# Optimization experiments

Hardware: AMD Instinct MI355X
Metric: run time of the kernel (lower is better)

Reference implementation:

```python
import jax, jax.numpy as jnp
import numpy as np

N = 50000            # problem dimension (free subspace)
K = 64               # low-rank dimension of the Hessian model
M = 64               # number of active equality constraints (rows of A)
MAX_CG_ITER = 40     # static bound on CG iterations -> reorth buffer size
CG_TOL = 1e-6
CG_REG = 1e-8
TOL_ABS = 1e-14      # _HRSTCG_TOL_ABS


def setup_inputs() -> dict:
    key = jax.random.key(0)
    k1, k2, k3, k4 = jax.random.split(key, 4)
    g_eff = jax.random.normal(k1, (N,), jnp.float32)
    # SPD diagonal part of the working Hessian: entries in [1, 2)
    diag = jax.random.uniform(k2, (N,), jnp.float32) + 1.0
    # low-rank factor, scaled so U U^T has O(1) spectrum
    U = jax.random.normal(k3, (N, K), jnp.float32) / np.float32(np.sqrt(N))
    # active constraint matrix, scaled so A A^T is well conditioned
    A = jax.random.normal(k4, (M, N), jnp.float32) / np.float32(np.sqrt(N))
    return {"g_eff": g_eff, "diag": diag, "U": U, "A": A}


def _hr_stcg(g_eff, diag, U, A):
    n = g_eff.shape[0]
    dtype = g_eff.dtype
    # exact null-space projector W(v) = v - A^T (A A^T)^{-1} A v
    AAt = A @ A.T + 1e-8 * jnp.eye(A.shape[0], dtype=A.dtype)
    AAt_inv = jnp.linalg.inv(AAt)
    project = lambda v: v - A.T @ (AAt_inv @ (A @ v))
    # working-subspace HVP: H v = diag*v + U (U^T v)  (SPD)
    hvp_work = lambda v: diag * v + U @ (U.T @ v)

    indices = jnp.arange(MAX_CG_ITER)

    Wg = project(g_eff)
    r0 = -Wg
    proj_grad_norm = jnp.sqrt(jnp.maximum(jnp.dot(r0, r0), 0.0))
    rz0 = jnp.dot(r0, r0)  # z0 = r0

    # state: (t, r, z, p, rz, P, HP, pHp_diag, iteration, converged)
    init_state = (
        jnp.zeros(n, dtype), r0, r0, r0, rz0,
        jnp.zeros((MAX_CG_ITER, n), dtype),
        jnp.zeros((MAX_CG_ITER, n), dtype),
        jnp.zeros(MAX_CG_ITER, dtype),
        jnp.array(0),
        jnp.reshape(proj_grad_norm <= TOL_ABS, ()),
    )

    def do_step(s):
        t, r, z, p, rz, P, HP, pHp_diag, it, conv = s
        Hp = hvp_work(p)
        pHp = jnp.dot(p, Hp)
        pp = jnp.dot(p, p)
        abs_floor = CG_REG * proj_grad_norm * proj_grad_norm
        bad_curvature = pHp <= jnp.maximum(CG_REG * pp, abs_floor)
        rp = jnp.dot(r, p)
        stagnation = jnp.abs(rp) < 1e-30
        sc = bad_curvature | stagnation  # short_circuit
        pHp_safe = jnp.maximum(pHp, 1e-30)
        alpha = jnp.where(sc, jnp.asarray(0.0, dtype), rz / pHp_safe)
        t_new = t + alpha * p
        r_new = r - alpha * Hp                 # modified residual recurrence
        z_new = project(r_new)
        P_buf = P.at[it].set(p)
        HP_buf = HP.at[it].set(Hp)
        pHp_buf = pHp_diag.at[it].set(pHp)
        mask_j = indices <= it
        Hz_dots = HP_buf @ z_new               # full H-conjugacy reorth
        pHp_diag_safe = jnp.where(jnp.abs(pHp_buf) > 1e-30, pHp_buf, 1e-30)
        coeffs = jnp.where(mask_j, Hz_dots / pHp_diag_safe, 0.0)
        p_new = z_new - coeffs @ P_buf
        rz_new = jnp.dot(r_new, z_new)
        z_norm = jnp.sqrt(jnp.maximum(jnp.dot(z_new, z_new), 0.0))
        tol_target = jnp.maximum(TOL_ABS, CG_TOL * proj_grad_norm)
        conv_new = (z_norm <= tol_target) | sc
        return (
            jnp.where(sc, t, t_new), jnp.where(sc, r, r_new),
            jnp.where(sc, z, z_new), jnp.where(sc, p, p_new),
            jnp.where(sc, rz, rz_new),
            P_buf, HP_buf, pHp_buf, it + 1, conv_new,
        )

    def step_fn(_i, s):
        return jax.lax.cond(jnp.reshape(s[-1], ()), lambda x: x, do_step, s)

    final = jax.lax.fori_loop(0, MAX_CG_ITER, step_fn, init_state)
    return final[0], proj_grad_norm, final[-1]


def reference(g_eff, diag, U, A):
    # returns (t_k, ||r0||, converged) as in _hr_stcg
    return _hr_stcg(g_eff, diag, U, A)
```

## Files before the change

kernel.cpp:

```cpp
#include <hip/hip_runtime.h>
#include <hip/hip_cooperative_groups.h>
#include <math.h>

namespace cg = cooperative_groups;

#define N_ 50000
#define K_ 64
#define M_ 64
#define MAXIT 40
#define NC 782
#define BSZ 256

#define CG_TOLf  1e-6f
#define CG_REGf  1e-8f
#define TOL_ABSf 1e-14f

#define OFF_AATB 0
#define OFF_INV  16384
#define OFF_S0   20480
#define OFF_AHP  20544
#define OFF_PGN2 23168
#define OFF_Y0   23680
#define OFF_BAR  56448
#define OFF_BUFA 57472
#define OFF_BUFB 230528
#define WS_HEAD  301184
#define OFF_PB   WS_HEAD
#define OFF_HPB  (OFF_PB + MAXIT * N_)

#define BUFA_SZ  86528
#define BUFB_SZ  35328

__device__ __forceinline__ float wred(float v) {
#pragma unroll
  for (int m = 1; m < 64; m <<= 1) v += __shfl_xor(v, m, 64);
  return v;
}

__device__ __forceinline__ void gbar(unsigned* bar, int b, int NB, unsigned ep) {
  __syncthreads();
  if (threadIdx.x == 0) {
    __threadfence();
    const int grp = b & 15;
    const unsigned gsz = (unsigned)((NB - grp + 15) >> 4);
    unsigned o = __hip_atomic_fetch_add(&bar[grp * 32], 1u, __ATOMIC_RELAXED, __HIP_MEMORY_SCOPE_AGENT);
    if (o % gsz == gsz - 1u) {
      unsigned r = __hip_atomic_fetch_add(&bar[16 * 32], 1u, __ATOMIC_RELAXED, __HIP_MEMORY_SCOPE_AGENT);
      if ((r & 15u) == 15u)
        __hip_atomic_fetch_add(&bar[17 * 32], 1u, __ATOMIC_RELEASE, __HIP_MEMORY_SCOPE_AGENT);
    }
    while (__hip_atomic_load(&bar[17 * 32], __ATOMIC_RELAXED, __HIP_MEMORY_SCOPE_AGENT) < ep)
      __builtin_amdgcn_s_sleep(2);
    __threadfence();
  }
  __syncthreads();
}

__device__ __forceinline__ void zslot(float* p, float v) {
  __hip_atomic_store(p, v, __ATOMIC_RELAXED, __HIP_MEMORY_SCOPE_AGENT);
}

__global__ __launch_bounds__(BSZ, 4)
void stcg_kernel(const float* __restrict__ g, const float* __restrict__ dg,
                 const float* __restrict__ U, const float* __restrict__ A,
                 float* __restrict__ out, float* __restrict__ ws)
{
  cg::grid_group grid = cg::this_grid();
  const int b = blockIdx.x, NB = gridDim.x, t = threadIdx.x;
  const int wv = t >> 6, lane = t & 63;
  const int base1 = b * 64;
  const int col1 = base1 + lane;
  const bool valid1 = col1 < N_;
  const bool own2 = (b + NB) < NC;
  const int base2 = (b + NB) * 64;
  const int col2 = base2 + lane;
  const bool valid2 = own2 && (col2 < N_);
  const int nv2 = own2 ? min(64, N_ - base2) : 0;
  const int bank32 = (b & 15) * 32;

  __shared__ float Als[64 * 65];
  __shared__ float Uls[64 * 65];
  __shared__ float partA[BSZ], partB[BSZ];
  __shared__ float rL[64], hpL[64], pL[64];
  __shared__ float rL2[64], hpL2[64], pL2[64];
  __shared__ float wsh[64], ssh[64], gL[64], cshL[64];
  __shared__ float rowk[64], fsh[64];
  __shared__ float redL[176];
  __shared__ float pHpdL[MAXIT];
  __shared__ float scalSh[8];

  float* Pb  = ws + OFF_PB;
  float* HPb = ws + OFF_HPB;
  unsigned* bar = (unsigned*)(ws + OFF_BAR);
  unsigned ep = 0;

  float t_ = 0.f, r_ = 0.f, p_ = 0.f, d_ = 0.f;
  float t2_ = 0.f, r2_ = 0.f, p2_ = 0.f, d2_ = 0.f;
  if (wv == 0 && valid1) d_ = dg[col1];
  if (wv == 1 && valid2) d2_ = dg[col2];

  for (int idx = b * BSZ + t; idx < WS_HEAD; idx += NB * BSZ) ws[idx] = 0.f;
  grid.sync();

  float aat[4][4];
#pragma unroll
  for (int a = 0; a < 4; ++a)
#pragma unroll
    for (int c = 0; c < 4; ++c) aat[a][c] = 0.f;
  const int tr4 = (t >> 4) << 2, tc4 = (t & 15) << 2;

  if (wv == 0) gL[lane] = valid1 ? g[col1] : 0.f;
#pragma unroll
  for (int kk = 0; kk < 16; ++kk) {
    const int m = wv * 16 + kk;
    Als[m * 65 + lane] = valid1 ? A[(size_t)m * N_ + col1] : 0.f;
  }
  __syncthreads();
  {
#pragma unroll 4
    for (int j = 0; j < 64; ++j) {
      float a0 = Als[(tr4 + 0) * 65 + j], a1 = Als[(tr4 + 1) * 65 + j];
      float a2 = Als[(tr4 + 2) * 65 + j], a3 = Als[(tr4 + 3) * 65 + j];
      float b0 = Als[(tc4 + 0) * 65 + j], b1 = Als[(tc4 + 1) * 65 + j];
      float b2 = Als[(tc4 + 2) * 65 + j], b3 = Als[(tc4 + 3) * 65 + j];
      aat[0][0] += a0 * b0; aat[0][1] += a0 * b1; aat[0][2] += a0 * b2; aat[0][3] += a0 * b3;
      aat[1][0] += a1 * b0; aat[1][1] += a1 * b1; aat[1][2] += a1 * b2; aat[1][3] += a1 * b3;
      aat[2][0] += a2 * b0; aat[2][1] += a2 * b1; aat[2][2] += a2 * b2; aat[2][3] += a2 * b3;
      aat[3][0] += a3 * b0; aat[3][1] += a3 * b1; aat[3][2] += a3 * b2; aat[3][3] += a3 * b3;
    }
    if (wv == 0) {
      float s = 0.f;
#pragma unroll 8
      for (int c = 0; c < 64; ++c) s += Als[lane * 65 + c] * gL[c];
      atomicAdd(&ws[OFF_Y0 + lane * 512 + bank32], s);
    }
  }
  if (own2) {
    __syncthreads();
    if (wv == 1) gL[lane] = valid2 ? g[col2] : 0.f;
#pragma unroll
    for (int kk = 0; kk < 16; ++kk) {
      const int m = wv * 16 + kk;
      Als[m * 65 + lane] = valid2 ? A[(size_t)m * N_ + col2] : 0.f;
    }
    __syncthreads();
#pragma unroll 4
    for (int j = 0; j < 64; ++j) {
      float a0 = Als[(tr4 + 0) * 65 + j], a1 = Als[(tr4 + 1) * 65 + j];
      float a2 = Als[(tr4 + 2) * 65 + j], a3 = Als[(tr4 + 3) * 65 + j];
      float b0 = Als[(tc4 + 0) * 65 + j], b1 = Als[(tc4 + 1) * 65 + j];
      float b2 = Als[(tc4 + 2) * 65 + j], b3 = Als[(tc4 + 3) * 65 + j];
      aat[0][0] += a0 * b0; aat[0][1] += a0 * b1; aat[0][2] += a0 * b2; aat[0][3] += a0 * b3;
      aat[1][0] += a1 * b0; aat[1][1] += a1 * b1; aat[1][2] += a1 * b2; aat[1][3] += a1 * b3;
      aat[2][0] += a2 * b0; aat[2][1] += a2 * b1; aat[2][2] += a2 * b2; aat[2][3] += a2 * b3;
      aat[3][0] += a3 * b0; aat[3][1] += a3 * b1; aat[3][2] += a3 * b2; aat[3][3] += a3 * b3;
    }
    if (wv == 1) {
      float s = 0.f;
#pragma unroll 8
      for (int c = 0; c < 64; ++c) s += Als[lane * 65 + c] * gL[c];
      atomicAdd(&ws[OFF_Y0 + lane * 512 + bank32], s);
    }
    __syncthreads();
#pragma unroll
    for (int kk = 0; kk < 16; ++kk) {
      const int m = wv * 16 + kk;
      Als[m * 65 + lane] = valid1 ? A[(size_t)m * N_ + col1] : 0.f;
    }
  }
  {
    float* bank = ws + OFF_AATB + (b & 3) * 4096;
#pragma unroll
    for (int a = 0; a < 4; ++a)
#pragma unroll
      for (int c = 0; c < 4; ++c)
        atomicAdd(&bank[(tr4 + a) * 64 + (tc4 + c)], aat[a][c]);
  }
  gbar(bar, b, NB, ++ep);

  if (b == 0) {
#pragma unroll
    for (int e = 0; e < 16; ++e) {
      const int idx = t * 16 + e;
      const int r = idx >> 6, c = idx & 63;
      float v = ws[OFF_AATB + idx] + ws[OFF_AATB + 4096 + idx] +
                ws[OFF_AATB + 8192 + idx] + ws[OFF_AATB + 12288 + idx];
      Uls[r * 65 + c] = v + ((r == c) ? 1e-8f : 0.f);
    }
    __syncthreads();
    for (int k = 0; k < 64; ++k) {
      if (t < 64) { rowk[t] = Uls[k * 65 + t]; fsh[t] = Uls[t * 65 + k]; }
      __syncthreads();
      const float piv = 1.0f / rowk[k];
      const int r = t & 63, q = t >> 6;
#pragma unroll
      for (int c2 = 0; c2 < 16; ++c2) {
        const int c = q * 16 + c2;
        const float rkc = rowk[c] * piv;
        float v;
        if (r == k) v = (c == k) ? piv : rkc;
        else        v = (c == k) ? (-fsh[r] * piv) : (Uls[r * 65 + c] - fsh[r] * rkc);
        Uls[r * 65 + c] = v;
      }
      __syncthreads();
    }
#pragma unroll
    for (int e = 0; e < 16; ++e) {
      const int idx = t * 16 + e;
      ws[OFF_INV + idx] = Uls[(idx >> 6) * 65 + (idx & 63)];
    }
    if (t < 64) {
      float a = 0.f;
#pragma unroll
      for (int k = 0; k < 16; ++k) a += ws[OFF_Y0 + t * 512 + k * 32];
      redL[t] = a;
    }
    __syncthreads();
    if (t < 64) {
      float s = 0.f;
#pragma unroll 8
      for (int j = 0; j < 64; ++j) s += Uls[t * 65 + j] * redL[j];
      ws[OFF_S0 + t] = s;
    }
    __syncthreads();
  }
  {
    const int row = t >> 2, q = t & 3;
    const int src = base1 + row;
#pragma unroll
    for (int jj = 0; jj < 4; ++jj) {
      const int k0 = q * 16 + 4 * jj;
      float4 u = make_float4(0.f, 0.f, 0.f, 0.f);
      if (src < N_) u = *reinterpret_cast<const float4*>(U + (size_t)src * K_ + k0);
      Uls[(k0 + 0) * 65 + row] = u.x;
      Uls[(k0 + 1) * 65 + row] = u.y;
      Uls[(k0 + 2) * 65 + row] = u.z;
      Uls[(k0 + 3) * 65 + row] = u.w;
    }
  }
  gbar(bar, b, NB, ++ep);

  if (t < 64) ssh[t] = ws[OFF_S0 + t];
  __syncthreads();
  {
    float* B0 = ws + OFF_BUFB;
    if (wv == 0) {
      float acc = 0.f;
#pragma unroll 8
      for (int m = 0; m < 64; ++m) acc += Als[m * 65 + lane] * ssh[m];
      float r0 = valid1 ? (acc - g[col1]) : 0.f;
      r_ = r0; p_ = r0; pL[lane] = r0;
      const float v  = wred(r0 * r0);
      const float v0 = wred(d_ * r0 * r0);
      if (lane == 0) {
        atomicAdd(&B0[(64 + 0) * 512 + bank32], v0);
        atomicAdd(&B0[(64 + 1) * 512 + bank32], v);
        atomicAdd(&B0[(64 + 2) * 512 + bank32], v);
        atomicAdd(&B0[(64 + 3) * 512 + bank32], v);
        atomicAdd(&B0[(64 + 4) * 512 + bank32], v);
        atomicAdd(&ws[OFF_PGN2 + bank32], v);
      }
    }
    if (wv == 1 && own2) {
      float acc = 0.f;
      if (valid2) {
#pragma unroll 8
        for (int m = 0; m < 64; ++m) acc += A[(size_t)m * N_ + col2] * ssh[m];
      }
      float r0 = valid2 ? (acc - g[col2]) : 0.f;
      r2_ = r0; p2_ = r0; pL2[lane] = r0;
      const float v  = wred(r0 * r0);
      const float v0 = wred(d2_ * r0 * r0);
      if (lane == 0) {
        atomicAdd(&B0[(64 + 0) * 512 + bank32], v0);
        atomicAdd(&B0[(64 + 1) * 512 + bank32], v);
        atomicAdd(&B0[(64 + 2) * 512 + bank32], v);
        atomicAdd(&B0[(64 + 3) * 512 + bank32], v);
        atomicAdd(&B0[(64 + 4) * 512 + bank32], v);
        atomicAdd(&ws[OFF_PGN2 + bank32], v);
      }
    }
    __syncthreads();
    if (wv == 0) {
      float s = 0.f;
#pragma unroll 8
      for (int c = 0; c < 64; ++c) s += Uls[lane * 65 + c] * pL[c];
      atomicAdd(&B0[lane * 512 + bank32], s);
    }
    if (wv == 1 && own2) {
      float s = 0.f;
      for (int c = 0; c < nv2; ++c) s += U[(size_t)(base2 + c) * K_ + lane] * pL2[c];
      atomicAdd(&B0[lane * 512 + bank32], s);
    }
  }
  gbar(bar, b, NB, ++ep);

  float pgn2v = 0.f;
#pragma unroll
  for (int k = 0; k < 16; ++k) pgn2v += ws[OFF_PGN2 + k * 32];
  const float pgn = sqrtf(fmaxf(pgn2v, 0.f));
  const float tolv = fmaxf(TOL_ABSf, CG_TOLf * pgn);
  bool sc_r = false, convf = false;

  for (int it = 0;; ++it) {
    const int p = it & 1;
    float* BB  = ws + OFF_BUFB + p * BUFB_SZ;
    float* BBn = ws + OFF_BUFB + (p ^ 1) * BUFB_SZ;
    float* BA  = ws + OFF_BUFA + p * BUFA_SZ;
    float* BAn = ws + OFF_BUFA + (p ^ 1) * BUFA_SZ;

    for (int line = t; line < 69; line += BSZ) {
      float a = 0.f;
#pragma unroll
      for (int k = 0; k < 16; ++k) a += BB[line * 512 + k * 32];
      if (line < 64) wsh[line] = a; else scalSh[line - 64] = a;
    }
    if (t < 4)
      for (int u = b * 4 + t; u < 69 * 16; u += NB * 4)
        zslot(&BBn[(u >> 4) * 512 + (u & 15) * 32], 0.f);
    __syncthreads();
    convf = sc_r || (sqrtf(fmaxf(scalSh[4], 0.f)) <= tolv);
    if (convf || it == MAXIT) break;

    const float pDp = scalSh[0], pp = scalSh[1], rp = scalSh[2], rz = scalSh[3];
    const float ww = wred(wsh[lane] * wsh[lane]);
    const float pHp = pDp + ww;
    const bool bad = pHp <= fmaxf(CG_REGf * pp, CG_REGf * pgn2v);
    sc_r = bad || (fabsf(rp) < 1e-30f);
    const float alpha = sc_r ? 0.f : rz / fmaxf(pHp, 1e-30f);
    if (t == 0) pHpdL[it] = pHp;

    {
      float acc = 0.f;
#pragma unroll
      for (int kk = 0; kk < 16; ++kk) {
        const int k = wv * 16 + kk;
        acc += Uls[k * 65 + lane] * wsh[k];
      }
      partA[t] = acc;
    }
    __syncthreads();
    if (wv == 0) {
      const float hp = d_ * p_ + partA[lane] + partA[64 + lane] + partA[128 + lane] + partA[192 + lane];
      t_ += alpha * p_;
      r_ -= alpha * hp;
      if (valid1) { Pb[(size_t)it * N_ + col1] = p_; HPb[(size_t)it * N_ + col1] = hp; }
      rL[lane] = r_; hpL[lane] = hp;
    }
    if (wv == 1 && own2) {
      float hp = d2_ * p2_;
      if (valid2) {
        const float4* Ur = reinterpret_cast<const float4*>(U + (size_t)col2 * K_);
#pragma unroll
        for (int k4 = 0; k4 < 16; ++k4) {
          float4 u = Ur[k4];
          hp += u.x * wsh[4 * k4 + 0] + u.y * wsh[4 * k4 + 1] + u.z * wsh[4 * k4 + 2] + u.w * wsh[4 * k4 + 3];
        }
      }
      t2_ += alpha * p2_;
      r2_ -= alpha * hp;
      if (valid2) { Pb[(size_t)it * N_ + col2] = p2_; HPb[(size_t)it * N_ + col2] = hp; }
      rL2[lane] = r2_; hpL2[lane] = hp;
    }
    __syncthreads();
    if (wv == 0) {
      float sy = 0.f, sa = 0.f;
#pragma unroll 8
      for (int c = 0; c < 64; ++c) {
        const float av = Als[lane * 65 + c];
        sy += av * rL[c];
        sa += av * hpL[c];
      }
      atomicAdd(&BA[lane * 512 + bank32], sy);
      atomicAdd(&BA[(64 + lane) * 512 + bank32], sa);
    } else if (wv == 1 && own2) {
      float sy = 0.f, sa = 0.f;
      for (int c = 0; c < nv2; ++c) {
        const float av = A[(size_t)lane * N_ + base2 + c];
        sy += av * rL2[c];
        sa += av * hpL2[c];
      }
      atomicAdd(&BA[lane * 512 + bank32], sy);
      atomicAdd(&BA[(64 + lane) * 512 + bank32], sa);
    }
    {
      const int hw0 = own2 ? 2 : 1;
      if (wv >= hw0) {
        const int nhw = 4 - hw0;
        for (int j = wv - hw0; j <= it; j += nhw) {
          float s = ((j == it) ? hpL[lane] : (valid1 ? HPb[(size_t)j * N_ + col1] : 0.f)) * rL[lane];
          if (own2) {
            const float hv2 = (j == it) ? hpL2[lane] : (valid2 ? HPb[(size_t)j * N_ + col2] : 0.f);
            s += hv2 * rL2[lane];
          }
          s = wred(s);
          if (lane == 0) atomicAdd(&BA[(128 + j) * 512 + bank32], s);
        }
      }
    }
    gbar(bar, b, NB, ++ep);

    const int nl = 129 + it;
    for (int line = t; line < nl; line += BSZ) {
      float a = 0.f;
#pragma unroll
      for (int k = 0; k < 16; ++k) a += BA[line * 512 + k * 32];
      redL[line] = a;
    }
    if (t < 4)
      for (int u = b * 4 + t; u < 169 * 16; u += NB * 4)
        zslot(&BAn[(u >> 4) * 512 + (u & 15) * 32], 0.f);
    __syncthreads();
    if (t < 64) {
      float s = 0.f;
      const float* invr = ws + OFF_INV + t * 64;
#pragma unroll 8
      for (int j = 0; j < 64; ++j) s += invr[j] * redL[j];
      ssh[t] = s;
    }
    if (b == 0 && t >= 64 && t < 128) ws[OFF_AHP + it * 64 + (t - 64)] = redL[t];
    __syncthreads();
    if (t < 64) {
      float c = 0.f;
      if (t <= it) {
        float hz = redL[128 + t];
        if (t == it) {
#pragma unroll 8
          for (int m = 0; m < 64; ++m) hz -= redL[64 + m] * ssh[m];
        } else {
          const float* ar = ws + OFF_AHP + t * 64;
#pragma unroll 8
          for (int m = 0; m < 64; ++m) hz -= ar[m] * ssh[m];
        }
        const float den = pHpdL[t];
        c = hz / ((fabsf(den) > 1e-30f) ? den : 1e-30f);
      }
      cshL[t] = c;
    }
    __syncthreads();
    {
      float accA = 0.f;
#pragma unroll
      for (int kk = 0; kk < 16; ++kk) {
        const int m = wv * 16 + kk;
        accA += Als[m * 65 + lane] * ssh[m];
      }
      partA[t] = accA;
      float accP = 0.f;
      for (int j = wv; j <= it; j += 4)
        accP += cshL[j] * (valid1 ? Pb[(size_t)j * N_ + col1] : 0.f);
      partB[t] = accP;
    }
    __syncthreads();
    if (wv == 0) {
      float z = r_ - (partA[lane] + partA[64 + lane] + partA[128 + lane] + partA[192 + lane]);
      float pn = z - (partB[lane] + partB[64 + lane] + partB[128 + lane] + partB[192 + lane]);
      if (!valid1) { z = 0.f; pn = 0.f; }
      p_ = pn; pL[lane] = pn;
      const float v0 = wred(d_ * pn * pn);
      const float v1 = wred(pn * pn);
      const float v2 = wred(r_ * pn);
      const float v3 = wred(r_ * z);
      const float v4 = wred(z * z);
      if (lane == 0) {
        atomicAdd(&BBn[(64 + 0) * 512 + bank32], v0);
        atomicAdd(&BBn[(64 + 1) * 512 + bank32], v1);
        atomicAdd(&BBn[(64 + 2) * 512 + bank32], v2);
        atomicAdd(&BBn[(64 + 3) * 512 + bank32], v3);
        atomicAdd(&BBn[(64 + 4) * 512 + bank32], v4);
      }
    }
    if (wv == 1 && own2) {
      float acc = 0.f, accP = 0.f;
      if (valid2) {
#pragma unroll 8
        for (int m = 0; m < 64; ++m) acc += A[(size_t)m * N_ + col2] * ssh[m];
        for (int j = 0; j <= it; ++j) accP += cshL[j] * Pb[(size_t)j * N_ + col2];
      }
      float z = r2_ - acc;
      float pn = z - accP;
      if (!valid2) { z = 0.f; pn = 0.f; }
      p2_ = pn; pL2[lane] = pn;
      const float v0 = wred(d2_ * pn * pn);
      const float v1 = wred(pn * pn);
      const float v2 = wred(r2_ * pn);
      const float v3 = wred(r2_ * z);
      const float v4 = wred(z * z);
      if (lane == 0) {
        atomicAdd(&BBn[(64 + 0) * 512 + bank32], v0);
        atomicAdd(&BBn[(64 + 1) * 512 + bank32], v1);
        atomicAdd(&BBn[(64 + 2) * 512 + bank32], v2);
        atomicAdd(&BBn[(64 + 3) * 512 + bank32], v3);
        atomicAdd(&BBn[(64 + 4) * 512 + bank32], v4);
      }
    }
    __syncthreads();
    if (wv == 0) {
      float s = 0.f;
#pragma unroll 8
      for (int c = 0; c < 64; ++c) s += Uls[lane * 65 + c] * pL[c];
      atomicAdd(&BBn[lane * 512 + bank32], s);
    }
    if (wv == 1 && own2) {
      float s = 0.f;
      for (int c = 0; c < nv2; ++c) s += U[(size_t)(base2 + c) * K_ + lane] * pL2[c];
      atomicAdd(&BBn[lane * 512 + bank32], s);
    }
    gbar(bar, b, NB, ++ep);
  }

  if (wv == 0 && valid1) out[col1] = t_;
  if (wv == 1 && valid2) out[col2] = t2_;
  if (b == 0 && t == 0) {
    out[N_]     = pgn;
    out[N_ + 1] = convf ? 1.f : 0.f;
  }
}

extern "C" void kernel_launch(void* const* d_in, const int* in_sizes, int n_in,
                              void* d_out, int out_size, void* d_ws, size_t ws_size,
                              hipStream_t stream) {
  (void)in_sizes; (void)n_in; (void)out_size; (void)ws_size;
  const float* g  = (const float*)d_in[0];
  const float* dg = (const float*)d_in[1];
  const float* U  = (const float*)d_in[2];
  const float* A  = (const float*)d_in[3];
  float* out = (float*)d_out;
  float* ws  = (float*)d_ws;

  int dev = 0;
  hipGetDevice(&dev);
  int nCU = 0;
  hipDeviceGetAttribute(&nCU, hipDeviceAttributeMultiprocessorCount, dev);
  if (nCU <= 0) nCU = 256;
  int maxB = 0;
  hipOccupancyMaxActiveBlocksPerMultiprocessor(&maxB, stcg_kernel, BSZ, 0);
  if (maxB <= 0) maxB = 1;
  int nblk = maxB * nCU;
  if (nblk > NC) nblk = NC;
  if (nblk < 391) nblk = 391;

  void* args[] = {(void*)&g, (void*)&dg, (void*)&U, (void*)&A, (void*)&out, (void*)&ws};
  hipLaunchCooperativeKernel(stcg_kernel, dim3(nblk), dim3(BSZ), args, 0, stream);
}
```

Baseline: 768.6 us.

## Compact reduction banks, keep inverse and U slices in registers, drop barrier fences

```diff
diff --git a/kernel.cpp b/kernel.cpp
--- a/kernel.cpp
+++ b/kernel.cpp
@@ -15,49 +15,60 @@
 #define CG_REGf  1e-8f
 #define TOL_ABSf 1e-14f
 
-#define OFF_AATB 0
-#define OFF_INV  16384
-#define OFF_S0   20480
-#define OFF_AHP  20544
-#define OFF_PGN2 23168
-#define OFF_Y0   23680
-#define OFF_BAR  56448
-#define OFF_BUFA 57472
-#define OFF_BUFB 230528
-#define WS_HEAD  301184
-#define OFF_PB   WS_HEAD
+#define OFF_Y0   0
+#define OFF_PGN2 2048
+#define OFF_S0   2080
+#define OFF_BAR  2144
+#define OFF_AATB 2720
+#define OFF_INV  19104
+#define OFF_BUFA 23200
+#define OFF_BUFB 34016
+#define WS_HEAD  38432
+#define OFF_PB   38464
 #define OFF_HPB  (OFF_PB + MAXIT * N_)
 
-#define BUFA_SZ  86528
-#define BUFB_SZ  35328
+#define BUFA_SZ  5408
+#define BUFB_SZ  2208
 
 __device__ __forceinline__ float wred(float v) {
 #pragma unroll
   for (int m = 1; m < 64; m <<= 1) v += __shfl_xor(v, m, 64);
   return v;
+}
+
+__device__ __forceinline__ float cload(const float* p) {
+  return __hip_atomic_load(p, __ATOMIC_RELAXED, __HIP_MEMORY_SCOPE_SYSTEM);
+}
+__device__ __forceinline__ void cstore(float* p, float v) {
+  __hip_atomic_store(p, v, __ATOMIC_RELAXED, __HIP_MEMORY_SCOPE_SYSTEM);
 }
 
 __device__ __forceinline__ void gbar(unsigned* bar, int b, int NB, unsigned ep) {
   __syncthreads();
   if (threadIdx.x == 0) {
-    __threadfence();
     const int grp = b & 15;
     const unsigned gsz = (unsigned)((NB - grp + 15) >> 4);
     unsigned o = __hip_atomic_fetch_add(&bar[grp * 32], 1u, __ATOMIC_RELAXED, __HIP_MEMORY_SCOPE_AGENT);
     if (o % gsz == gsz - 1u) {
       unsigned r = __hip_atomic_fetch_add(&bar[16 * 32], 1u, __ATOMIC_RELAXED, __HIP_MEMORY_SCOPE_AGENT);
       if ((r & 15u) == 15u)
-        __hip_atomic_fetch_add(&bar[17 * 32], 1u, __ATOMIC_RELEASE, __HIP_MEMORY_SCOPE_AGENT);
-    }
-    while (__hip_atomic_load(&bar[17 * 32], __ATOMIC_RELAXED, __HIP_MEMORY_SCOPE_AGENT) < ep)
+        __hip_atomic_fetch_add(&bar[17 * 32], 1u, __ATOMIC_RELAXED, __HIP_MEMORY_SCOPE_AGENT);
+    }
+    while (__hip_atomic_load(&bar[17 * 32], __ATOMIC_RELAXED, __HIP_MEMORY_SCOPE_SYSTEM) < ep)
       __builtin_amdgcn_s_sleep(2);
-    __threadfence();
   }
   __syncthreads();
 }
 
-__device__ __forceinline__ void zslot(float* p, float v) {
-  __hip_atomic_store(p, v, __ATOMIC_RELAXED, __HIP_MEMORY_SCOPE_AGENT);
+__device__ __forceinline__ void consume(const float* buf, int nl, float* dst, int t) {
+  const int wv = t >> 6, lane = t & 63;
+  const int half = lane >> 5, bk = lane & 31;
+  for (int l = wv * 2 + half; l < nl; l += 8) {
+    float v = cload(&buf[l * 32 + bk]);
+#pragma unroll
+    for (int m = 1; m < 32; m <<= 1) v += __shfl_xor(v, m, 64);
+    if (bk == 0) dst[l] = v;
+  }
 }
 
 __global__ __launch_bounds__(BSZ, 4)
@@ -76,18 +87,17 @@
   const int col2 = base2 + lane;
   const bool valid2 = own2 && (col2 < N_);
   const int nv2 = own2 ? min(64, N_ - base2) : 0;
-  const int bank32 = (b & 15) * 32;
+  const int bank = b & 31;
 
   __shared__ float Als[64 * 65];
-  __shared__ float Uls[64 * 65];
-  __shared__ float partA[BSZ], partB[BSZ];
+  __shared__ float AHPl[41 * 65];
+  __shared__ float partA[BSZ];
   __shared__ float rL[64], hpL[64], pL[64];
   __shared__ float rL2[64], hpL2[64], pL2[64];
-  __shared__ float wsh[64], ssh[64], gL[64], cshL[64];
+  __shared__ float ssh[64], cshL[64];
   __shared__ float rowk[64], fsh[64];
-  __shared__ float redL[176];
+  __shared__ float redL[184];
   __shared__ float pHpdL[MAXIT];
-  __shared__ float scalSh[8];
 
   float* Pb  = ws + OFF_PB;
   float* HPb = ws + OFF_HPB;
@@ -96,6 +106,8 @@
 
   float t_ = 0.f, r_ = 0.f, p_ = 0.f, d_ = 0.f;
   float t2_ = 0.f, r2_ = 0.f, p2_ = 0.f, d2_ = 0.f;
+  float invr[16];
+  float ur[16];
   if (wv == 0 && valid1) d_ = dg[col1];
   if (wv == 1 && valid2) d2_ = dg[col2];
 
@@ -109,7 +121,7 @@
     for (int c = 0; c < 4; ++c) aat[a][c] = 0.f;
   const int tr4 = (t >> 4) << 2, tc4 = (t & 15) << 2;
 
-  if (wv == 0) gL[lane] = valid1 ? g[col1] : 0.f;
+  if (wv == 0) cshL[lane] = valid1 ? g[col1] : 0.f;
 #pragma unroll
   for (int kk = 0; kk < 16; ++kk) {
     const int m = wv * 16 + kk;
@@ -131,13 +143,13 @@
     if (wv == 0) {
       float s = 0.f;
 #pragma unroll 8
-      for (int c = 0; c < 64; ++c) s += Als[lane * 65 + c] * gL[c];
-      atomicAdd(&ws[OFF_Y0 + lane * 512 + bank32], s);
+      for (int c = 0; c < 64; ++c) s += Als[lane * 65 + c] * cshL[c];
+      atomicAdd(&ws[OFF_Y0 + lane * 32 + bank], s);
     }
   }
   if (own2) {
     __syncthreads();
-    if (wv == 1) gL[lane] = valid2 ? g[col2] : 0.f;
+    if (wv == 1) cshL[lane] = valid2 ? g[col2] : 0.f;
 #pragma unroll
     for (int kk = 0; kk < 16; ++kk) {
       const int m = wv * 16 + kk;
@@ -158,8 +170,8 @@
     if (wv == 1) {
       float s = 0.f;
 #pragma unroll 8
-      for (int c = 0; c < 64; ++c) s += Als[lane * 65 + c] * gL[c];
-      atomicAdd(&ws[OFF_Y0 + lane * 512 + bank32], s);
+      for (int c = 0; c < 64; ++c) s += Als[lane * 65 + c] * cshL[c];
+      atomicAdd(&ws[OFF_Y0 + lane * 32 + bank], s);
     }
     __syncthreads();
 #pragma unroll
@@ -169,78 +181,85 @@
     }
   }
   {
-    float* bank = ws + OFF_AATB + (b & 3) * 4096;
+    float* bk4 = ws + OFF_AATB + (b & 3) * 4096;
 #pragma unroll
     for (int a = 0; a < 4; ++a)
 #pragma unroll
       for (int c = 0; c < 4; ++c)
-        atomicAdd(&bank[(tr4 + a) * 64 + (tc4 + c)], aat[a][c]);
+        atomicAdd(&bk4[(tr4 + a) * 64 + (tc4 + c)], aat[a][c]);
   }
   gbar(bar, b, NB, ++ep);
 
   if (b == 0) {
 #pragma unroll
-    for (int e = 0; e < 16; ++e) {
-      const int idx = t * 16 + e;
-      const int r = idx >> 6, c = idx & 63;
-      float v = ws[OFF_AATB + idx] + ws[OFF_AATB + 4096 + idx] +
-                ws[OFF_AATB + 8192 + idx] + ws[OFF_AATB + 12288 + idx];
-      Uls[r * 65 + c] = v + ((r == c) ? 1e-8f : 0.f);
+    for (int kk = 0; kk < 16; ++kk) {
+      const int idx = lane * 64 + wv * 16 + kk;
+      float v = cload(&ws[OFF_AATB + idx]) + cload(&ws[OFF_AATB + 4096 + idx]) +
+                cload(&ws[OFF_AATB + 8192 + idx]) + cload(&ws[OFF_AATB + 12288 + idx]);
+      invr[kk] = v + ((lane == wv * 16 + kk) ? 1e-8f : 0.f);
     }
     __syncthreads();
     for (int k = 0; k < 64; ++k) {
-      if (t < 64) { rowk[t] = Uls[k * 65 + t]; fsh[t] = Uls[t * 65 + k]; }
+      if (lane == k) {
+#pragma unroll
+        for (int kk = 0; kk < 16; ++kk) rowk[wv * 16 + kk] = invr[kk];
+      }
+      if (wv == (k >> 4)) fsh[lane] = invr[k & 15];
       __syncthreads();
       const float piv = 1.0f / rowk[k];
-      const int r = t & 63, q = t >> 6;
-#pragma unroll
-      for (int c2 = 0; c2 < 16; ++c2) {
-        const int c = q * 16 + c2;
+      const float fr = fsh[lane];
+#pragma unroll
+      for (int kk = 0; kk < 16; ++kk) {
+        const int c = wv * 16 + kk;
         const float rkc = rowk[c] * piv;
         float v;
-        if (r == k) v = (c == k) ? piv : rkc;
-        else        v = (c == k) ? (-fsh[r] * piv) : (Uls[r * 65 + c] - fsh[r] * rkc);
-        Uls[r * 65 + c] = v;
+        if (lane == k) v = (c == k) ? piv : rkc;
+        else           v = (c == k) ? (-fr * piv) : (invr[kk] - fr * rkc);
+        invr[kk] = v;
       }
       __syncthreads();
     }
 #pragma unroll
-    for (int e = 0; e < 16; ++e) {
-      const int idx = t * 16 + e;
-      ws[OFF_INV + idx] = Uls[(idx >> 6) * 65 + (idx & 63)];
-    }
+    for (int kk = 0; kk < 16; ++kk)
+      cstore(&ws[OFF_INV + lane * 64 + wv * 16 + kk], invr[kk]);
     if (t < 64) {
       float a = 0.f;
 #pragma unroll
-      for (int k = 0; k < 16; ++k) a += ws[OFF_Y0 + t * 512 + k * 32];
+      for (int k2 = 0; k2 < 32; ++k2) a += cload(&ws[OFF_Y0 + t * 32 + k2]);
       redL[t] = a;
     }
     __syncthreads();
-    if (t < 64) {
-      float s = 0.f;
-#pragma unroll 8
-      for (int j = 0; j < 64; ++j) s += Uls[t * 65 + j] * redL[j];
-      ws[OFF_S0 + t] = s;
-    }
-    __syncthreads();
+    {
+      float ps = 0.f;
+#pragma unroll
+      for (int kk = 0; kk < 16; ++kk) ps += invr[kk] * redL[wv * 16 + kk];
+      partA[t] = ps;
+    }
+    __syncthreads();
+    if (t < 64) cstore(&ws[OFF_S0 + t], partA[t] + partA[64 + t] + partA[128 + t] + partA[192 + t]);
   }
   {
-    const int row = t >> 2, q = t & 3;
-    const int src = base1 + row;
-#pragma unroll
-    for (int jj = 0; jj < 4; ++jj) {
-      const int k0 = q * 16 + 4 * jj;
-      float4 u = make_float4(0.f, 0.f, 0.f, 0.f);
-      if (src < N_) u = *reinterpret_cast<const float4*>(U + (size_t)src * K_ + k0);
-      Uls[(k0 + 0) * 65 + row] = u.x;
-      Uls[(k0 + 1) * 65 + row] = u.y;
-      Uls[(k0 + 2) * 65 + row] = u.z;
-      Uls[(k0 + 3) * 65 + row] = u.w;
+    if (valid1) {
+      const float4* Up = reinterpret_cast<const float4*>(U + (size_t)col1 * K_ + wv * 16);
+      float4 u0 = Up[0], u1 = Up[1], u2 = Up[2], u3 = Up[3];
+      ur[0]=u0.x; ur[1]=u0.y; ur[2]=u0.z; ur[3]=u0.w;
+      ur[4]=u1.x; ur[5]=u1.y; ur[6]=u1.z; ur[7]=u1.w;
+      ur[8]=u2.x; ur[9]=u2.y; ur[10]=u2.z; ur[11]=u2.w;
+      ur[12]=u3.x; ur[13]=u3.y; ur[14]=u3.z; ur[15]=u3.w;
+    } else {
+#pragma unroll
+      for (int kk = 0; kk < 16; ++kk) ur[kk] = 0.f;
     }
   }
   gbar(bar, b, NB, ++ep);
 
-  if (t < 64) ssh[t] = ws[OFF_S0 + t];
+  if (b != 0) {
+#pragma unroll
+    for (int kk = 0; kk < 16; ++kk)
+      invr[kk] = cload(&ws[OFF_INV + lane * 64 + wv * 16 + kk]);
+  }
+
+  if (t < 64) ssh[t] = cload(&ws[OFF_S0 + t]);
   __syncthreads();
   {
     float* B0 = ws + OFF_BUFB;
@@ -253,12 +272,12 @@
       const float v  = wred(r0 * r0);
       const float v0 = wred(d_ * r0 * r0);
       if (lane == 0) {
-        atomicAdd(&B0[(64 + 0) * 512 + bank32], v0);
-        atomicAdd(&B0[(64 + 1) * 512 + bank32], v);
-        atomicAdd(&B0[(64 + 2) * 512 + bank32], v);
-        atomicAdd(&B0[(64 + 3) * 512 + bank32], v);
-        atomicAdd(&B0[(64 + 4) * 512 + bank32], v);
-        atomicAdd(&ws[OFF_PGN2 + bank32], v);
+        atomicAdd(&B0[(64 + 0) * 32 + bank], v0);
+        atomicAdd(&B0[(64 + 1) * 32 + bank], v);
+        atomicAdd(&B0[(64 + 2) * 32 + bank], v);
+        atomicAdd(&B0[(64 + 3) * 32 + bank], v);
+        atomicAdd(&B0[(64 + 4) * 32 + bank], v);
+        atomicAdd(&ws[OFF_PGN2 + bank], v);
       }
     }
     if (wv == 1 && own2) {
@@ -272,32 +291,31 @@
       const float v  = wred(r0 * r0);
       const float v0 = wred(d2_ * r0 * r0);
       if (lane == 0) {
-        atomicAdd(&B0[(64 + 0) * 512 + bank32], v0);
-        atomicAdd(&B0[(64 + 1) * 512 + bank32], v);
-        atomicAdd(&B0[(64 + 2) * 512 + bank32], v);
-        atomicAdd(&B0[(64 + 3) * 512 + bank32], v);
-        atomicAdd(&B0[(64 + 4) * 512 + bank32], v);
-        atomicAdd(&ws[OFF_PGN2 + bank32], v);
-      }
-    }
-    __syncthreads();
-    if (wv == 0) {
-      float s = 0.f;
-#pragma unroll 8
-      for (int c = 0; c < 64; ++c) s += Uls[lane * 65 + c] * pL[c];
-      atomicAdd(&B0[lane * 512 + bank32], s);
+        atomicAdd(&B0[(64 + 0) * 32 + bank], v0);
+        atomicAdd(&B0[(64 + 1) * 32 + bank], v);
+        atomicAdd(&B0[(64 + 2) * 32 + bank], v);
+        atomicAdd(&B0[(64 + 3) * 32 + bank], v);
+        atomicAdd(&B0[(64 + 4) * 32 + bank], v);
+        atomicAdd(&ws[OFF_PGN2 + bank], v);
+      }
+    }
+    __syncthreads();
+#pragma unroll
+    for (int kk = 0; kk < 16; ++kk) {
+      const float s = wred(ur[kk] * pL[lane]);
+      if (lane == 0) atomicAdd(&B0[(wv * 16 + kk) * 32 + bank], s);
     }
     if (wv == 1 && own2) {
       float s = 0.f;
       for (int c = 0; c < nv2; ++c) s += U[(size_t)(base2 + c) * K_ + lane] * pL2[c];
-      atomicAdd(&B0[lane * 512 + bank32], s);
+      atomicAdd(&B0[lane * 32 + bank], s);
     }
   }
   gbar(bar, b, NB, ++ep);
 
   float pgn2v = 0.f;
 #pragma unroll
-  for (int k = 0; k < 16; ++k) pgn2v += ws[OFF_PGN2 + k * 32];
+  for (int k = 0; k < 32; ++k) pgn2v += cload(&ws[OFF_PGN2 + k]);
   const float pgn = sqrtf(fmaxf(pgn2v, 0.f));
   const float tolv = fmaxf(TOL_ABSf, CG_TOLf * pgn);
   bool sc_r = false, convf = false;
@@ -309,21 +327,14 @@
     float* BA  = ws + OFF_BUFA + p * BUFA_SZ;
     float* BAn = ws + OFF_BUFA + (p ^ 1) * BUFA_SZ;
 
-    for (int line = t; line < 69; line += BSZ) {
-      float a = 0.f;
-#pragma unroll
-      for (int k = 0; k < 16; ++k) a += BB[line * 512 + k * 32];
-      if (line < 64) wsh[line] = a; else scalSh[line - 64] = a;
-    }
-    if (t < 4)
-      for (int u = b * 4 + t; u < 69 * 16; u += NB * 4)
-        zslot(&BBn[(u >> 4) * 512 + (u & 15) * 32], 0.f);
-    __syncthreads();
-    convf = sc_r || (sqrtf(fmaxf(scalSh[4], 0.f)) <= tolv);
+    consume(BB, 69, redL, t);
+    for (int u = b * BSZ + t; u < BUFB_SZ; u += NB * BSZ) cstore(&BBn[u], 0.f);
+    __syncthreads();
+    const float pDp = redL[64], pp = redL[65], rp = redL[66], rz = redL[67], zz = redL[68];
+    convf = sc_r || (sqrtf(fmaxf(zz, 0.f)) <= tolv);
     if (convf || it == MAXIT) break;
 
-    const float pDp = scalSh[0], pp = scalSh[1], rp = scalSh[2], rz = scalSh[3];
-    const float ww = wred(wsh[lane] * wsh[lane]);
+    const float ww = wred(redL[lane] * redL[lane]);
     const float pHp = pDp + ww;
     const bool bad = pHp <= fmaxf(CG_REGf * pp, CG_REGf * pgn2v);
     sc_r = bad || (fabsf(rp) < 1e-30f);
@@ -333,10 +344,7 @@
     {
       float acc = 0.f;
 #pragma unroll
-      for (int kk = 0; kk < 16; ++kk) {
-        const int k = wv * 16 + kk;
-        acc += Uls[k * 65 + lane] * wsh[k];
-      }
+      for (int kk = 0; kk < 16; ++kk) acc += ur[kk] * redL[wv * 16 + kk];
       partA[t] = acc;
     }
     __syncthreads();
@@ -350,11 +358,11 @@
     if (wv == 1 && own2) {
       float hp = d2_ * p2_;
       if (valid2) {
-        const float4* Ur = reinterpret_cast<const float4*>(U + (size_t)col2 * K_);
+        const float4* Urow = reinterpret_cast<const float4*>(U + (size_t)col2 * K_);
 #pragma unroll
         for (int k4 = 0; k4 < 16; ++k4) {
-          float4 u = Ur[k4];
-          hp += u.x * wsh[4 * k4 + 0] + u.y * wsh[4 * k4 + 1] + u.z * wsh[4 * k4 + 2] + u.w * wsh[4 * k4 + 3];
+          float4 u = Urow[k4];
+          hp += u.x * redL[4 * k4 + 0] + u.y * redL[4 * k4 + 1] + u.z * redL[4 * k4 + 2] + u.w * redL[4 * k4 + 3];
         }
       }
       t2_ += alpha * p2_;
@@ -371,8 +379,8 @@
         sy += av * rL[c];
         sa += av * hpL[c];
       }
-      atomicAdd(&BA[lane * 512 + bank32], sy);
-      atomicAdd(&BA[(64 + lane) * 512 + bank32], sa);
+      atomicAdd(&BA[lane * 32 + bank], sy);
+      atomicAdd(&BA[(64 + lane) * 32 + bank], sa);
     } else if (wv == 1 && own2) {
       float sy = 0.f, sa = 0.f;
       for (int c = 0; c < nv2; ++c) {
@@ -380,8 +388,8 @@
         sy += av * rL2[c];
         sa += av * hpL2[c];
       }
-      atomicAdd(&BA[lane * 512 + bank32], sy);
-      atomicAdd(&BA[(64 + lane) * 512 + bank32], sa);
+      atomicAdd(&BA[lane * 32 + bank], sy);
+      atomicAdd(&BA[(64 + lane) * 32 + bank], sa);
     }
     {
       const int hw0 = own2 ? 2 : 1;
@@ -394,44 +402,32 @@
             s += hv2 * rL2[lane];
           }
           s = wred(s);
-          if (lane == 0) atomicAdd(&BA[(128 + j) * 512 + bank32], s);
+          if (lane == 0) atomicAdd(&BA[(128 + j) * 32 + bank], s);
         }
       }
     }
     gbar(bar, b, NB, ++ep);
 
-    const int nl = 129 + it;
-    for (int line = t; line < nl; line += BSZ) {
-      float a = 0.f;
-#pragma unroll
-      for (int k = 0; k < 16; ++k) a += BA[line * 512 + k * 32];
-      redL[line] = a;
-    }
-    if (t < 4)
-      for (int u = b * 4 + t; u < 169 * 16; u += NB * 4)
-        zslot(&BAn[(u >> 4) * 512 + (u & 15) * 32], 0.f);
-    __syncthreads();
-    if (t < 64) {
-      float s = 0.f;
-      const float* invr = ws + OFF_INV + t * 64;
-#pragma unroll 8
-      for (int j = 0; j < 64; ++j) s += invr[j] * redL[j];
-      ssh[t] = s;
-    }
-    if (b == 0 && t >= 64 && t < 128) ws[OFF_AHP + it * 64 + (t - 64)] = redL[t];
+    consume(BA, 129 + it, redL, t);
+    for (int u = b * BSZ + t; u < BUFA_SZ; u += NB * BSZ) cstore(&BAn[u], 0.f);
+    __syncthreads();
+    if (t < 64) AHPl[it * 65 + t] = redL[64 + t];
+    {
+      float ps = 0.f;
+#pragma unroll
+      for (int kk = 0; kk < 16; ++kk) ps += invr[kk] * redL[wv * 16 + kk];
+      partA[t] = ps;
+    }
+    __syncthreads();
+    if (t < 64) ssh[t] = partA[t] + partA[64 + t] + partA[128 + t] + partA[192 + t];
     __syncthreads();
     if (t < 64) {
       float c = 0.f;
       if (t <= it) {
         float hz = redL[128 + t];
-        if (t == it) {
-#pragma unroll 8
-          for (int m = 0; m < 64; ++m) hz -= redL[64 + m] * ssh[m];
-        } else {
-          const float* ar = ws + OFF_AHP + t * 64;
-#pragma unroll 8
-          for (int m = 0; m < 64; ++m) hz -= ar[m] * ssh[m];
-        }
+        const float* ar = AHPl + t * 65;
+#pragma unroll 8
+        for (int m = 0; m < 64; ++m) hz -= ar[m] * ssh[m];
         const float den = pHpdL[t];
         c = hz / ((fabsf(den) > 1e-30f) ? den : 1e-30f);
       }
@@ -446,16 +442,34 @@
         accA += Als[m * 65 + lane] * ssh[m];
       }
       partA[t] = accA;
-      float accP = 0.f;
-      for (int j = wv; j <= it; j += 4)
-        accP += cshL[j] * (valid1 ? Pb[(size_t)j * N_ + col1] : 0.f);
-      partB[t] = accP;
     }
     __syncthreads();
     if (wv == 0) {
       float z = r_ - (partA[lane] + partA[64 + lane] + partA[128 + lane] + partA[192 + lane]);
-      float pn = z - (partB[lane] + partB[64 + lane] + partB[128 + lane] + partB[192 + lane]);
-      if (!valid1) { z = 0.f; pn = 0.f; }
+      if (!valid1) z = 0.f;
+      hpL[lane] = z;
+    }
+    if (wv == 1 && own2) {
+      float acc = 0.f;
+      if (valid2) {
+#pragma unroll 8
+        for (int m = 0; m < 64; ++m) acc += A[(size_t)m * N_ + col2] * ssh[m];
+      }
+      hpL2[lane] = valid2 ? (r2_ - acc) : 0.f;
+    }
+    __syncthreads();
+    {
+      float accP = 0.f;
+      if (valid1) {
+        for (int j = wv; j <= it; j += 4) accP += cshL[j] * Pb[(size_t)j * N_ + col1];
+      }
+      partA[t] = accP;
+    }
+    __syncthreads();
+    if (wv == 0) {
+      const float z = hpL[lane];
+      float pn = z - (partA[lane] + partA[64 + lane] + partA[128 + lane] + partA[192 + lane]);
+      if (!valid1) pn = 0.f;
       p_ = pn; pL[lane] = pn;
       const float v0 = wred(d_ * pn * pn);
       const float v1 = wred(pn * pn);
@@ -463,48 +477,44 @@
       const float v3 = wred(r_ * z);
       const float v4 = wred(z * z);
       if (lane == 0) {
-        atomicAdd(&BBn[(64 + 0) * 512 + bank32], v0);
-        atomicAdd(&BBn[(64 + 1) * 512 + bank32], v1);
-        atomicAdd(&BBn[(64 + 2) * 512 + bank32], v2);
-        atomicAdd(&BBn[(64 + 3) * 512 + bank32], v3);
-        atomicAdd(&BBn[(64 + 4) * 512 + bank32], v4);
+        atomicAdd(&BBn[(64 + 0) * 32 + bank], v0);
+        atomicAdd(&BBn[(64 + 1) * 32 + bank], v1);
+        atomicAdd(&BBn[(64 + 2) * 32 + bank], v2);
+        atomicAdd(&BBn[(64 + 3) * 32 + bank], v3);
+        atomicAdd(&BBn[(64 + 4) * 32 + bank], v4);
       }
     }
     if (wv == 1 && own2) {
-      float acc = 0.f, accP = 0.f;
+      const float z2 = hpL2[lane];
+      float accP2 = 0.f;
       if (valid2) {
-#pragma unroll 8
-        for (int m = 0; m < 64; ++m) acc += A[(size_t)m * N_ + col2] * ssh[m];
-        for (int j = 0; j <= it; ++j) accP += cshL[j] * Pb[(size_t)j * N_ + col2];
-      }
-      float z = r2_ - acc;
-      float pn = z - accP;
-      if (!valid2) { z = 0.f; pn = 0.f; }
+        for (int j = 0; j <= it; ++j) accP2 += cshL[j] * Pb[(size_t)j * N_ + col2];
+      }
+      float pn = valid2 ? (z2 - accP2) : 0.f;
       p2_ = pn; pL2[lane] = pn;
       const float v0 = wred(d2_ * pn * pn);
       const float v1 = wred(pn * pn);
       const float v2 = wred(r2_ * pn);
-      const float v3 = wred(r2_ * z);
-      const float v4 = wred(z * z);
+      const float v3 = wred(r2_ * z2);
+      const float v4 = wred(z2 * z2);
       if (lane == 0) {
-        atomicAdd(&BBn[(64 + 0) * 512 + bank32], v0);
-        atomicAdd(&BBn[(64 + 1) * 512 + bank32], v1);
-        atomicAdd(&BBn[(64 + 2) * 512 + bank32], v2);
-        atomicAdd(&BBn[(64 + 3) * 512 + bank32], v3);
-        atomicAdd(&BBn[(64 + 4) * 512 + bank32], v4);
-      }
-    }
-    __syncthreads();
-    if (wv == 0) {
-      float s = 0.f;
-#pragma unroll 8
-      for (int c = 0; c < 64; ++c) s += Uls[lane * 65 + c] * pL[c];
-      atomicAdd(&BBn[lane * 512 + bank32], s);
+        atomicAdd(&BBn[(64 + 0) * 32 + bank], v0);
+        atomicAdd(&BBn[(64 + 1) * 32 + bank], v1);
+        atomicAdd(&BBn[(64 + 2) * 32 + bank], v2);
+        atomicAdd(&BBn[(64 + 3) * 32 + bank], v3);
+        atomicAdd(&BBn[(64 + 4) * 32 + bank], v4);
+      }
+    }
+    __syncthreads();
+#pragma unroll
+    for (int kk = 0; kk < 16; ++kk) {
+      const float s = wred(ur[kk] * pL[lane]);
+      if (lane == 0) atomicAdd(&BBn[(wv * 16 + kk) * 32 + bank], s);
     }
     if (wv == 1 && own2) {
       float s = 0.f;
       for (int c = 0; c < nv2; ++c) s += U[(size_t)(base2 + c) * K_ + lane] * pL2[c];
-      atomicAdd(&BBn[lane * 512 + bank32], s);
+      atomicAdd(&BBn[lane * 32 + bank], s);
     }
     gbar(bar, b, NB, ++ep);
   }
```

New measurement: 671.4 us. 1.14x faster.
